# Performance work log

Measured on AMD Instinct MI355X. Metric: run time of the kernel, lower is better.

The kernel has to match this reference:

```python
import jax, jax.numpy as jnp
import numpy as np

N_NODES = 100000
NUM_REL = 2


def rgcn_conv(x, src, dst, etype, W, root, bias):
    """PyG-style RGCNConv: per-relation mean aggregation + root transform + bias.
    x: [N, in], W: [R, in, out], root: [in, out], bias: [out].
    """
    R = W.shape[0]
    N = x.shape[0]
    # Pre-transform nodes by every relation weight: [R, N, out]
    xr = jnp.einsum('ni,rio->rno', x, W)
    msgs = xr[etype, src]  # [E, out] gather per-edge, relation-typed
    seg_id = dst * R + etype  # combined (node, relation) segment id
    summed = jax.ops.segment_sum(msgs, seg_id, num_segments=N * R)
    cnt = jax.ops.segment_sum(jnp.ones(etype.shape, x.dtype), seg_id, num_segments=N * R)
    summed = summed.reshape(N, R, -1)
    cnt = cnt.reshape(N, R, 1)
    agg = (summed / jnp.maximum(cnt, 1.0)).sum(axis=1)  # sum over relations of per-relation means
    return agg + x @ root + bias


def setup_inputs() -> dict:
    key = jax.random.key(0)
    ks = jax.random.split(key, 9)
    d = 128
    E = 800000
    sc = 1.0 / np.sqrt(d)
    return {
        'x': jax.random.normal(ks[0], (N_NODES, d), jnp.float32),
        'edge_index_a': jax.random.randint(ks[1], (2, E), 0, N_NODES, jnp.int64),
        'edge_index_b': jax.random.randint(ks[2], (2, E), 0, N_NODES, jnp.int64),
        'W1': jax.random.normal(ks[3], (NUM_REL, d, d), jnp.float32) * sc,
        'root1': jax.random.normal(ks[4], (d, d), jnp.float32) * sc,
        'b1': jnp.zeros((d,), jnp.float32),
        'W2': jax.random.normal(ks[5], (NUM_REL, d, d), jnp.float32) * sc,
        'root2': jax.random.normal(ks[6], (d, d), jnp.float32) * sc,
        'b2': jnp.zeros((d,), jnp.float32),
    }


def reference(x, edge_index_a, edge_index_b, W1, root1, b1, W2, root2, b2):
    # Concatenate per-relation edge lists + build edge_type ids (a->0, b->1)
    edge_index = jnp.concatenate([edge_index_a, edge_index_b], axis=1)
    etype = jnp.concatenate([
        jnp.zeros((edge_index_a.shape[1],), jnp.int32),
        jnp.ones((edge_index_b.shape[1],), jnp.int32),
    ])
    src, dst = edge_index[0], edge_index[1]
    h = rgcn_conv(x, src, dst, etype, W1, root1, b1)
    h = jax.nn.relu(h)
    out = rgcn_conv(h, src, dst, etype, W2, root2, b2)
    return out
```

## Files before the change

kernel.cpp:

```cpp
#include <hip/hip_runtime.h>
#include <hip/hip_bf16.h>


typedef __attribute__((ext_vector_type(8))) short bf16x8;
typedef __attribute__((ext_vector_type(4))) float f32x4;
typedef unsigned short ushort_t;
typedef unsigned int uint_t;

#define BSHIFT 9
#define SEGB (1 << (BSHIFT + 1))
#define NBMAX 256
#define SLAB 16384
#define CH_PER_THREAD 8
#define CHUNK (256 * CH_PER_THREAD)
#define XSB 1024

#define GBM 256
#define KCH 128
#define LDBE 136

#define ROWB 768
#define XOFF 512

__device__ __forceinline__ ushort_t f2b(float f) {
  union { float f; uint_t u; } v;
  v.f = f;
  uint_t u = v.u;
  return (ushort_t)((u + 0x7FFFu + ((u >> 16) & 1u)) >> 16);
}
__device__ __forceinline__ void dot2acc(float& a, uint_t pk, uint_t sel) {
  asm("v_dot2_f32_bf16 %0, %1, %2, %0" : "+v"(a) : "v"(pk), "v"(sel));
}

__global__ __launch_bounds__(256) void prep_bin(
    const int* __restrict__ ea, const int* __restrict__ eb, int E, int NB,
    int* __restrict__ cursor, uint_t* __restrict__ staging, int nchunk,
    const float* __restrict__ W1, const float* __restrict__ root1,
    const float* __restrict__ W2, const float* __restrict__ root2,
    ushort_t* __restrict__ Bt1, ushort_t* __restrict__ Bt2,
    const float* __restrict__ x, ushort_t* __restrict__ aggbuf1, int N) {
  __shared__ int h[NBMAX];
  __shared__ int bbase[NBMAX];
  __shared__ int lofs[NBMAX];
  __shared__ int wtot[4];
  __shared__ uint_t sval[CHUNK];
  __shared__ int sdst[CHUNK];
  int b = blockIdx.x;
  int t = threadIdx.x;

  if (b < nchunk) {
    for (int i = t; i < NB; i += 256) h[i] = 0;
    __syncthreads();
    int base_i = b * CHUNK + t * CH_PER_THREAD;
    int total = 2 * E;
    int srcv[CH_PER_THREAD], dstv[CH_PER_THREAD], relv;
    bool valid8 = false;
    if (base_i + CH_PER_THREAD <= E) {
      int4 s0 = *(const int4*)(ea + base_i);
      int4 s1 = *(const int4*)(ea + base_i + 4);
      int4 d0 = *(const int4*)(ea + E + base_i);
      int4 d1 = *(const int4*)(ea + E + base_i + 4);
      srcv[0]=s0.x; srcv[1]=s0.y; srcv[2]=s0.z; srcv[3]=s0.w;
      srcv[4]=s1.x; srcv[5]=s1.y; srcv[6]=s1.z; srcv[7]=s1.w;
      dstv[0]=d0.x; dstv[1]=d0.y; dstv[2]=d0.z; dstv[3]=d0.w;
      dstv[4]=d1.x; dstv[5]=d1.y; dstv[6]=d1.z; dstv[7]=d1.w;
      relv = 0; valid8 = true;
    } else if (base_i >= E && base_i + CH_PER_THREAD <= total) {
      int off = base_i - E;
      int4 s0 = *(const int4*)(eb + off);
      int4 s1 = *(const int4*)(eb + off + 4);
      int4 d0 = *(const int4*)(eb + E + off);
      int4 d1 = *(const int4*)(eb + E + off + 4);
      srcv[0]=s0.x; srcv[1]=s0.y; srcv[2]=s0.z; srcv[3]=s0.w;
      srcv[4]=s1.x; srcv[5]=s1.y; srcv[6]=s1.z; srcv[7]=s1.w;
      dstv[0]=d0.x; dstv[1]=d0.y; dstv[2]=d0.z; dstv[3]=d0.w;
      dstv[4]=d1.x; dstv[5]=d1.y; dstv[6]=d1.z; dstv[7]=d1.w;
      relv = 1; valid8 = true;
    }
    uint_t val[CH_PER_THREAD];
    short bktv[CH_PER_THREAD];
    short rj[CH_PER_THREAD];
    if (valid8) {
#pragma unroll
      for (int j = 0; j < CH_PER_THREAD; ++j) {
        int seg = dstv[j] * 2 + relv;
        int bkt = seg >> (BSHIFT + 1);
        val[j] = ((uint_t)srcv[j] << 10) | (uint_t)(seg & (SEGB - 1));
        bktv[j] = (short)bkt;
        rj[j] = (short)atomicAdd(&h[bkt], 1);
      }
    } else {
#pragma unroll
      for (int j = 0; j < CH_PER_THREAD; ++j) {
        int i = base_i + j;
        if (i < total) {
          int src, dst, rel;
          if (i < E) { src = ea[i];     dst = ea[E + i]; rel = 0; }
          else       { src = eb[i - E]; dst = eb[i];     rel = 1; }
          int seg = dst * 2 + rel;
          int bkt = seg >> (BSHIFT + 1);
          val[j] = ((uint_t)src << 10) | (uint_t)(seg & (SEGB - 1));
          bktv[j] = (short)bkt;
          rj[j] = (short)atomicAdd(&h[bkt], 1);
        } else {
          bktv[j] = -1;
        }
      }
    }
    __syncthreads();
    {
      int v = (t < NB) ? h[t] : 0;
      int lane = t & 63, w = t >> 6;
      int s = v;
#pragma unroll
      for (int off = 1; off < 64; off <<= 1) {
        int u = __shfl_up(s, off);
        if (lane >= off) s += u;
      }
      if (lane == 63) wtot[w] = s;
      __syncthreads();
      int woff = 0;
#pragma unroll
      for (int i = 0; i < 4; ++i)
        if (i < w) woff += wtot[i];
      int incl = s + woff;
      if (t < NB) {
        lofs[t] = incl - v;
        bbase[t] = v ? t * SLAB + atomicAdd(&cursor[t], v) : 0;
      }
    }
    __syncthreads();
#pragma unroll
    for (int j = 0; j < CH_PER_THREAD; ++j) {
      if (!valid8 && bktv[j] < 0) continue;
      int bkt = bktv[j];
      int pos = lofs[bkt] + rj[j];
      sval[pos] = val[j];
      sdst[pos] = bbase[bkt] + rj[j];
    }
    __syncthreads();
    int nrec = 2 * E - b * CHUNK;
    if (nrec > CHUNK) nrec = CHUNK;
    for (int i = t; i < nrec; i += 256)
      staging[sdst[i]] = sval[i];
  } else if (b < nchunk + 384) {
    int flat = (b - nchunk) * 256 + t;
    int which = flat >= 49152;
    int idx = flat - which * 49152;
    int c = idx / 384;
    int k = idx - c * 384;
    const float* W = which ? W2 : W1;
    const float* root = which ? root2 : root1;
    ushort_t* Bt = which ? Bt2 : Bt1;
    float v = (k < 256) ? W[(size_t)k * 128 + c] : root[(size_t)(k - 256) * 128 + c];
    Bt[(size_t)c * 384 + k] = f2b(v);
  } else {
    int idx = (b - nchunk - 384) * 256 + t;
    int tot = N * 16;
    int step = XSB * 256;
    for (; idx < tot; idx += step) {
      int n = idx >> 4, tq = idx & 15;
      float4 a = *(const float4*)(x + (size_t)n * 128 + tq * 8);
      float4 c = *(const float4*)(x + (size_t)n * 128 + tq * 8 + 4);
      uint4 o;
      o.x = (uint_t)f2b(a.x) | ((uint_t)f2b(a.y) << 16);
      o.y = (uint_t)f2b(a.z) | ((uint_t)f2b(a.w) << 16);
      o.z = (uint_t)f2b(c.x) | ((uint_t)f2b(c.y) << 16);
      o.w = (uint_t)f2b(c.z) | ((uint_t)f2b(c.w) << 16);
      *(uint4*)(aggbuf1 + (size_t)n * 384 + 256 + tq * 8) = o;
    }
  }
}

__global__ __launch_bounds__(1024) void bucket_build(
    const uint_t* __restrict__ staging, const int* __restrict__ cursor,
    int* __restrict__ csr, int* __restrict__ offs,
    int* __restrict__ ends, int nseg) {
  __shared__ int scnt[SEGB];
  __shared__ int sexcl[SEGB];
  __shared__ int wtot[16];
  int b = blockIdx.x;
  int t = threadIdx.x;
  int base = b * SLAB;
  int ne = cursor[b];
  int seg0 = b << (BSHIFT + 1);

  scnt[t] = 0;
  __syncthreads();
  const uint_t* st = staging + base;
  uint_t rec[16];
  short rk[16];
#pragma unroll
  for (int k = 0; k < 4; ++k) {
    int i = (t + k * 1024) * 4;
    if (i + 4 <= ne) {
      uint4 v = *(const uint4*)(st + i);
      rec[k * 4 + 0] = v.x;
      rec[k * 4 + 1] = v.y;
      rec[k * 4 + 2] = v.z;
      rec[k * 4 + 3] = v.w;
#pragma unroll
      for (int j = 0; j < 4; ++j)
        rk[k * 4 + j] = (short)atomicAdd(&scnt[rec[k * 4 + j] & (SEGB - 1)], 1);
    } else {
#pragma unroll
      for (int j = 0; j < 4; ++j) {
        int i2 = i + j;
        if (i2 < ne) {
          uint_t v = st[i2];
          rec[k * 4 + j] = v;
          rk[k * 4 + j] = (short)atomicAdd(&scnt[v & (SEGB - 1)], 1);
        } else {
          rec[k * 4 + j] = 0xffffffffu;
        }
      }
    }
  }
  __syncthreads();
  int c = scnt[t];
  {
    int lane = t & 63, w = t >> 6;
    int s = c;
#pragma unroll
    for (int off = 1; off < 64; off <<= 1) {
      int u = __shfl_up(s, off);
      if (lane >= off) s += u;
    }
    if (lane == 63) wtot[w] = s;
    __syncthreads();
    int woff = 0;
#pragma unroll
    for (int i = 0; i < 16; ++i)
      if (i < w) woff += wtot[i];
    int excl = s + woff - c;
    sexcl[t] = excl;
    int g = seg0 + t;
    if (g < nseg) { offs[g] = base + excl; ends[g] = base + excl + c; }
  }
  __syncthreads();
#pragma unroll
  for (int k = 0; k < 16; ++k) {
    if (rec[k] != 0xffffffffu) {
      int seg = (int)(rec[k] & (SEGB - 1));
      int src = (int)(rec[k] >> 10);
      csr[base + sexcl[seg] + rk[k]] = src * ROWB + XOFF;
    }
  }
}

__global__ __launch_bounds__(256) void agg_kernel(
    const char* __restrict__ xbc,
    const int* __restrict__ csr,
    const int* __restrict__ offs, const int* __restrict__ ends,
    ushort_t* __restrict__ agg, int nseg) {
  int wid = (blockIdx.x * blockDim.x + threadIdx.x) >> 6;
  if (wid >= nseg) return;
  int lane = threadIdx.x & 63;
  int q = lane >> 4;
  int t = lane & 15;
  int beg = offs[wid], end = ends[wid];
  const uint_t sel_lo = 0x00003F80u;
  const uint_t sel_hi = 0x3F800000u;

  float acc[8];
#pragma unroll
  for (int j = 0; j < 8; ++j) acc[j] = 0.f;

  const char* xt = xbc + t * 16;
  int e = beg + q;
  for (; e + 4 < end; e += 8) {
    int o0 = csr[e];
    int o1 = csr[e + 4];
    uint4 v0 = *(const uint4*)(xt + o0);
    uint4 v1 = *(const uint4*)(xt + o1);
    dot2acc(acc[0], v0.x, sel_lo); dot2acc(acc[1], v0.x, sel_hi);
    dot2acc(acc[2], v0.y, sel_lo); dot2acc(acc[3], v0.y, sel_hi);
    dot2acc(acc[4], v0.z, sel_lo); dot2acc(acc[5], v0.z, sel_hi);
    dot2acc(acc[6], v0.w, sel_lo); dot2acc(acc[7], v0.w, sel_hi);
    dot2acc(acc[0], v1.x, sel_lo); dot2acc(acc[1], v1.x, sel_hi);
    dot2acc(acc[2], v1.y, sel_lo); dot2acc(acc[3], v1.y, sel_hi);
    dot2acc(acc[4], v1.z, sel_lo); dot2acc(acc[5], v1.z, sel_hi);
    dot2acc(acc[6], v1.w, sel_lo); dot2acc(acc[7], v1.w, sel_hi);
  }
  if (e < end) {
    int o0 = csr[e];
    uint4 v0 = *(const uint4*)(xt + o0);
    dot2acc(acc[0], v0.x, sel_lo); dot2acc(acc[1], v0.x, sel_hi);
    dot2acc(acc[2], v0.y, sel_lo); dot2acc(acc[3], v0.y, sel_hi);
    dot2acc(acc[4], v0.z, sel_lo); dot2acc(acc[5], v0.z, sel_hi);
    dot2acc(acc[6], v0.w, sel_lo); dot2acc(acc[7], v0.w, sel_hi);
  }

#pragma unroll
  for (int j = 0; j < 8; ++j) {
    acc[j] += __shfl_xor(acc[j], 16);
    acc[j] += __shfl_xor(acc[j], 32);
  }

  int c = end - beg;
  float inv = 1.0f / (float)(c > 1 ? c : 1);
  if (q == 0) {
    uint4 o;
    o.x = (uint_t)f2b(acc[0] * inv) | ((uint_t)f2b(acc[1] * inv) << 16);
    o.y = (uint_t)f2b(acc[2] * inv) | ((uint_t)f2b(acc[3] * inv) << 16);
    o.z = (uint_t)f2b(acc[4] * inv) | ((uint_t)f2b(acc[5] * inv) << 16);
    o.w = (uint_t)f2b(acc[6] * inv) | ((uint_t)f2b(acc[7] * inv) << 16);
    int n = wid >> 1, r = wid & 1;
    *(uint4*)(agg + (size_t)n * 384 + r * 128 + t * 8) = o;
  }
}

__device__ __forceinline__ void do_mfma32(
    const char* bs, f32x4 (&acc)[4][8], const bf16x8 (&a)[4],
    int ks, int lrow, int kg) {
  bf16x8 b[8];
#pragma unroll
  for (int c = 0; c < 8; ++c)
    b[c] = *(const bf16x8*)(bs + (c * 16 + lrow) * (LDBE * 2) +
                            (ks * 4 + kg) * 16);
#pragma unroll
  for (int r = 0; r < 4; ++r)
#pragma unroll
    for (int c = 0; c < 8; ++c)
      acc[r][c] = __builtin_amdgcn_mfma_f32_16x16x32_bf16(a[r], b[c], acc[r][c], 0, 0, 0);
}

template <int MODE>
__global__ __launch_bounds__(256, 2) void mfma_gemm(
    const ushort_t* __restrict__ A,
    const ushort_t* __restrict__ Bt,
    const float* __restrict__ bias,
    float* __restrict__ outf,
    ushort_t* __restrict__ outb,
    int M) {
  __shared__ __align__(16) ushort_t Bs[2][128 * LDBE];
  const int tid = threadIdx.x;
  const int lane = tid & 63;
  const int wave = tid >> 6;
  const int lrow = lane & 15;
  const int kg = lane >> 4;
  const int rowbase = blockIdx.x * GBM + wave * 64;

  f32x4 acc[4][8];
#pragma unroll
  for (int r = 0; r < 4; ++r)
#pragma unroll
    for (int c = 0; c < 8; ++c) acc[r][c] = (f32x4){0.f, 0.f, 0.f, 0.f};

  uint4 stg[8];
#pragma unroll
  for (int j = 0; j < 8; ++j) {
    int flat = tid + j * 256;
    int col = flat >> 4;
    int q = flat & 15;
    stg[j] = *(const uint4*)(Bt + (size_t)col * 384 + q * 8);
  }
#pragma unroll
  for (int j = 0; j < 8; ++j) {
    int flat = tid + j * 256;
    int col = flat >> 4;
    int q = flat & 15;
    *(uint4*)((char*)&Bs[0][0] + col * (LDBE * 2) + q * 16) = stg[j];
  }
  __syncthreads();

  int cur = 0;
  for (int ch = 0; ch < 3; ++ch) {
    if (ch < 2) {
#pragma unroll
      for (int j = 0; j < 8; ++j) {
        int flat = tid + j * 256;
        int col = flat >> 4;
        int q = flat & 15;
        stg[j] = *(const uint4*)(Bt + (size_t)col * 384 + (ch + 1) * KCH + q * 8);
      }
    }
    const ushort_t* ab = A + (size_t)ch * KCH + kg * 8;
    const char* bsbase = (const char*)&Bs[0][0] + cur * (128 * LDBE * 2);
    bf16x8 aA[4], aB[4];
#pragma unroll
    for (int r = 0; r < 4; ++r)
      aA[r] = *(const bf16x8*)(ab + (size_t)(rowbase + r * 16 + lrow) * 384);
#pragma unroll
    for (int r = 0; r < 4; ++r)
      aB[r] = *(const bf16x8*)(ab + (size_t)(rowbase + r * 16 + lrow) * 384 + 32);
    do_mfma32(bsbase, acc, aA, 0, lrow, kg);
#pragma unroll
    for (int r = 0; r < 4; ++r)
      aA[r] = *(const bf16x8*)(ab + (size_t)(rowbase + r * 16 + lrow) * 384 + 64);
    do_mfma32(bsbase, acc, aB, 1, lrow, kg);
#pragma unroll
    for (int r = 0; r < 4; ++r)
      aB[r] = *(const bf16x8*)(ab + (size_t)(rowbase + r * 16 + lrow) * 384 + 96);
    do_mfma32(bsbase, acc, aA, 2, lrow, kg);
    do_mfma32(bsbase, acc, aB, 3, lrow, kg);
    if (ch < 2) {
#pragma unroll
      for (int j = 0; j < 8; ++j) {
        int flat = tid + j * 256;
        int col = flat >> 4;
        int q = flat & 15;
        *(uint4*)((char*)&Bs[0][0] + (cur ^ 1) * (128 * LDBE * 2) +
                  col * (LDBE * 2) + q * 16) = stg[j];
      }
      __syncthreads();
      cur ^= 1;
    }
  }

  if (MODE == 1) {
    __syncthreads();
    ushort_t* ws = (ushort_t*)&Bs[0][0] + wave * (64 * 128);
#pragma unroll
    for (int c = 0; c < 8; ++c) {
      int col = c * 16 + lrow;
      float bv = bias[col];
#pragma unroll
      for (int r = 0; r < 4; ++r)
#pragma unroll
        for (int j = 0; j < 4; ++j) {
          float v = fmaxf(acc[r][c][j] + bv, 0.f);
          ws[(r * 16 + kg * 4 + j) * 128 + col] = f2b(v);
        }
    }
    __syncthreads();
#pragma unroll
    for (int rr = 0; rr < 16; ++rr) {
      int lr = rr * 4 + (lane >> 4);
      int row = rowbase + lr;
      int tq = lane & 15;
      if (row < M) {
        uint4 v = *(const uint4*)(ws + lr * 128 + tq * 8);
        *(uint4*)(outb + (size_t)row * 384 + 256 + tq * 8) = v;
      }
    }
  } else {
#pragma unroll
    for (int c = 0; c < 8; ++c) {
      int col = c * 16 + lrow;
      float bv = bias[col];
#pragma unroll
      for (int r = 0; r < 4; ++r) {
        int r0 = rowbase + r * 16 + kg * 4;
#pragma unroll
        for (int j = 0; j < 4; ++j) {
          int row = r0 + j;
          if (row < M) {
            outf[(size_t)row * 128 + col] = acc[r][c][j] + bv;
          }
        }
      }
    }
  }
}

extern "C" void kernel_launch(void* const* d_in, const int* in_sizes, int n_in,
                              void* d_out, int out_size, void* d_ws, size_t ws_size,
                              hipStream_t stream) {
  const float* x     = (const float*)d_in[0];
  const int*   ea    = (const int*)d_in[1];
  const int*   eb    = (const int*)d_in[2];
  const float* W1    = (const float*)d_in[3];
  const float* root1 = (const float*)d_in[4];
  const float* b1    = (const float*)d_in[5];
  const float* W2    = (const float*)d_in[6];
  const float* root2 = (const float*)d_in[7];
  const float* b2    = (const float*)d_in[8];
  float* out = (float*)d_out;

  const int N = in_sizes[0] / 128;
  const int E = in_sizes[1] / 2;
  const int nseg = N * 2;
  const int Mblk = (N + GBM - 1) / GBM;
  const int Mpad = Mblk * GBM;
  const int NB = ((N - 1) >> BSHIFT) + 1;
  const int nchunk = (2 * E + CHUNK - 1) / CHUNK;

  char* p = (char*)d_ws;
  ushort_t* aggbuf1 = (ushort_t*)p;  p += (size_t)Mpad * 384 * sizeof(ushort_t);
  ushort_t* aggbuf2 = (ushort_t*)p;  p += (size_t)Mpad * 384 * sizeof(ushort_t);
  ushort_t* Bt1 = (ushort_t*)p;      p += (size_t)128 * 384 * sizeof(ushort_t);
  ushort_t* Bt2 = (ushort_t*)p;      p += (size_t)128 * 384 * sizeof(ushort_t);
  int* csr = (int*)p;                p += (size_t)NBMAX * SLAB * sizeof(int);
  int* offs = (int*)p;               p += (size_t)nseg * sizeof(int);
  int* ends = (int*)p;               p += (size_t)nseg * sizeof(int);
  int* cursor = (int*)p;             p += NBMAX * sizeof(int);
  uint_t* staging = (uint_t*)aggbuf2;

  hipMemsetAsync(cursor, 0, NBMAX * sizeof(int), stream);

  prep_bin<<<nchunk + 384 + XSB, 256, 0, stream>>>(
      ea, eb, E, NB, cursor, staging, nchunk,
      W1, root1, W2, root2, Bt1, Bt2, x, aggbuf1, N);

  bucket_build<<<NB, 1024, 0, stream>>>(staging, cursor, csr, offs, ends, nseg);

  const int agg_blocks = (nseg + 3) / 4;

  agg_kernel<<<agg_blocks, 256, 0, stream>>>((const char*)aggbuf1, csr, offs,
                                             ends, aggbuf1, nseg);
  mfma_gemm<1><<<Mblk, 256, 0, stream>>>(aggbuf1, Bt1, b1, nullptr, aggbuf2, N);

  agg_kernel<<<agg_blocks, 256, 0, stream>>>((const char*)aggbuf2, csr, offs,
                                             ends, aggbuf2, nseg);
  mfma_gemm<0><<<Mblk, 256, 0, stream>>>(aggbuf2, Bt2, b2, out, nullptr, N);
}
```

Measured before the change: 288.2 us.

## Store activations in column-sliced layout so gathers hit a compact per-slice working set

Changes the bf16 activation/aggregation buffer from row-major [N,384] to 24 column slices of 16 features each, stored [slice][node][32 bytes]. The aggregation kernel now assigns each block to one slice, so concurrent blocks gather from a 3.2 MB slice that can stay cache-resident instead of scattering across the full 77 MB buffer. Each segment is now handled by 8 lanes instead of a 64-lane wave. The GEMM A-loads and epilogue stores are rewritten for the new layout. The cost is that each segment's CSR indices are re-read once per slice, and GEMM A-loads now stride across slices.

```diff
diff --git a/kernel.cpp b/kernel.cpp
--- a/kernel.cpp
+++ b/kernel.cpp
@@ -19,9 +19,6 @@
 #define KCH 128
 #define LDBE 136
 
-#define ROWB 768
-#define XOFF 512
-
 __device__ __forceinline__ ushort_t f2b(float f) {
   union { float f; uint_t u; } v;
   v.f = f;
@@ -31,6 +28,11 @@
 __device__ __forceinline__ void dot2acc(float& a, uint_t pk, uint_t sel) {
   asm("v_dot2_f32_bf16 %0, %1, %2, %0" : "+v"(a) : "v"(pk), "v"(sel));
 }
+#define ACC8(v)                                               \
+  dot2acc(acc[0], v.x, sel_lo); dot2acc(acc[1], v.x, sel_hi); \
+  dot2acc(acc[2], v.y, sel_lo); dot2acc(acc[3], v.y, sel_hi); \
+  dot2acc(acc[4], v.z, sel_lo); dot2acc(acc[5], v.z, sel_hi); \
+  dot2acc(acc[6], v.w, sel_lo); dot2acc(acc[7], v.w, sel_hi);
 
 __global__ __launch_bounds__(256) void prep_bin(
     const int* __restrict__ ea, const int* __restrict__ eb, int E, int NB,
@@ -38,7 +40,7 @@
     const float* __restrict__ W1, const float* __restrict__ root1,
     const float* __restrict__ W2, const float* __restrict__ root2,
     ushort_t* __restrict__ Bt1, ushort_t* __restrict__ Bt2,
-    const float* __restrict__ x, ushort_t* __restrict__ aggbuf1, int N) {
+    const float* __restrict__ x, char* __restrict__ A1, int N, int Mpad) {
   __shared__ int h[NBMAX];
   __shared__ int bbase[NBMAX];
   __shared__ int lofs[NBMAX];
@@ -155,6 +157,7 @@
     float v = (k < 256) ? W[(size_t)k * 128 + c] : root[(size_t)(k - 256) * 128 + c];
     Bt[(size_t)c * 384 + k] = f2b(v);
   } else {
+    size_t Mstride = (size_t)Mpad * 32;
     int idx = (b - nchunk - 384) * 256 + t;
     int tot = N * 16;
     int step = XSB * 256;
@@ -167,7 +170,8 @@
       o.y = (uint_t)f2b(a.z) | ((uint_t)f2b(a.w) << 16);
       o.z = (uint_t)f2b(c.x) | ((uint_t)f2b(c.y) << 16);
       o.w = (uint_t)f2b(c.z) | ((uint_t)f2b(c.w) << 16);
-      *(uint4*)(aggbuf1 + (size_t)n * 384 + 256 + tq * 8) = o;
+      *(uint4*)(A1 + (size_t)(16 + (tq >> 1)) * Mstride + (size_t)n * 32 +
+                (tq & 1) * 16) = o;
     }
   }
 }
@@ -243,22 +247,25 @@
     if (rec[k] != 0xffffffffu) {
       int seg = (int)(rec[k] & (SEGB - 1));
       int src = (int)(rec[k] >> 10);
-      csr[base + sexcl[seg] + rk[k]] = src * ROWB + XOFF;
+      csr[base + sexcl[seg] + rk[k]] = src * 32;
     }
   }
 }
 
 __global__ __launch_bounds__(256) void agg_kernel(
-    const char* __restrict__ xbc,
+    const char* __restrict__ Ain,
+    char* __restrict__ Aout,
     const int* __restrict__ csr,
     const int* __restrict__ offs, const int* __restrict__ ends,
-    ushort_t* __restrict__ agg, int nseg) {
-  int wid = (blockIdx.x * blockDim.x + threadIdx.x) >> 6;
-  if (wid >= nseg) return;
-  int lane = threadIdx.x & 63;
-  int q = lane >> 4;
-  int t = lane & 15;
-  int beg = offs[wid], end = ends[wid];
+    int nseg, int Mpad) {
+  size_t Mstride = (size_t)Mpad * 32;
+  int slice = blockIdx.x & 7;
+  int widx = (blockIdx.x >> 3) * 32 + (threadIdx.x >> 3);
+  if (widx >= nseg) return;
+  int l = threadIdx.x & 7;
+  int es = l >> 1;
+  int hb = l & 1;
+  int beg = offs[widx], end = ends[widx];
   const uint_t sel_lo = 0x00003F80u;
   const uint_t sel_hi = 0x3F800000u;
 
@@ -266,47 +273,38 @@
 #pragma unroll
   for (int j = 0; j < 8; ++j) acc[j] = 0.f;
 
-  const char* xt = xbc + t * 16;
-  int e = beg + q;
+  const char* xt = Ain + (size_t)(16 + slice) * Mstride + hb * 16;
+  int e = beg + es;
   for (; e + 4 < end; e += 8) {
     int o0 = csr[e];
     int o1 = csr[e + 4];
     uint4 v0 = *(const uint4*)(xt + o0);
     uint4 v1 = *(const uint4*)(xt + o1);
-    dot2acc(acc[0], v0.x, sel_lo); dot2acc(acc[1], v0.x, sel_hi);
-    dot2acc(acc[2], v0.y, sel_lo); dot2acc(acc[3], v0.y, sel_hi);
-    dot2acc(acc[4], v0.z, sel_lo); dot2acc(acc[5], v0.z, sel_hi);
-    dot2acc(acc[6], v0.w, sel_lo); dot2acc(acc[7], v0.w, sel_hi);
-    dot2acc(acc[0], v1.x, sel_lo); dot2acc(acc[1], v1.x, sel_hi);
-    dot2acc(acc[2], v1.y, sel_lo); dot2acc(acc[3], v1.y, sel_hi);
-    dot2acc(acc[4], v1.z, sel_lo); dot2acc(acc[5], v1.z, sel_hi);
-    dot2acc(acc[6], v1.w, sel_lo); dot2acc(acc[7], v1.w, sel_hi);
+    ACC8(v0); ACC8(v1);
   }
   if (e < end) {
     int o0 = csr[e];
     uint4 v0 = *(const uint4*)(xt + o0);
-    dot2acc(acc[0], v0.x, sel_lo); dot2acc(acc[1], v0.x, sel_hi);
-    dot2acc(acc[2], v0.y, sel_lo); dot2acc(acc[3], v0.y, sel_hi);
-    dot2acc(acc[4], v0.z, sel_lo); dot2acc(acc[5], v0.z, sel_hi);
-    dot2acc(acc[6], v0.w, sel_lo); dot2acc(acc[7], v0.w, sel_hi);
+    ACC8(v0);
   }
 
 #pragma unroll
   for (int j = 0; j < 8; ++j) {
-    acc[j] += __shfl_xor(acc[j], 16);
-    acc[j] += __shfl_xor(acc[j], 32);
+    acc[j] += __shfl_xor(acc[j], 2);
+    acc[j] += __shfl_xor(acc[j], 4);
   }
 
   int c = end - beg;
   float inv = 1.0f / (float)(c > 1 ? c : 1);
-  if (q == 0) {
+  if (es == 0) {
     uint4 o;
     o.x = (uint_t)f2b(acc[0] * inv) | ((uint_t)f2b(acc[1] * inv) << 16);
     o.y = (uint_t)f2b(acc[2] * inv) | ((uint_t)f2b(acc[3] * inv) << 16);
     o.z = (uint_t)f2b(acc[4] * inv) | ((uint_t)f2b(acc[5] * inv) << 16);
     o.w = (uint_t)f2b(acc[6] * inv) | ((uint_t)f2b(acc[7] * inv) << 16);
-    int n = wid >> 1, r = wid & 1;
-    *(uint4*)(agg + (size_t)n * 384 + r * 128 + t * 8) = o;
+    int n = widx >> 1, r = widx & 1;
+    *(uint4*)(Aout + (size_t)(r * 8 + slice) * Mstride + (size_t)n * 32 +
+              hb * 16) = o;
   }
 }
 
@@ -325,15 +323,21 @@
       acc[r][c] = __builtin_amdgcn_mfma_f32_16x16x32_bf16(a[r], b[c], acc[r][c], 0, 0, 0);
 }
 
+#define ALOAD(r, koff)                                                        \
+  (*(const bf16x8*)(Ap + (size_t)(((ch * KCH + (koff)) >> 4) + (kg >> 1)) *   \
+                             Mstride +                                        \
+                    (size_t)(rowbase + (r) * 16 + lrow) * 32 + (kg & 1) * 16))
+
 template <int MODE>
 __global__ __launch_bounds__(256, 2) void mfma_gemm(
-    const ushort_t* __restrict__ A,
+    const char* __restrict__ Ap,
     const ushort_t* __restrict__ Bt,
     const float* __restrict__ bias,
     float* __restrict__ outf,
-    ushort_t* __restrict__ outb,
-    int M) {
+    char* __restrict__ outb,
+    int M, int Mpad) {
   __shared__ __align__(16) ushort_t Bs[2][128 * LDBE];
+  size_t Mstride = (size_t)Mpad * 32;
   const int tid = threadIdx.x;
   const int lane = tid & 63;
   const int wave = tid >> 6;
@@ -375,23 +379,18 @@
         stg[j] = *(const uint4*)(Bt + (size_t)col * 384 + (ch + 1) * KCH + q * 8);
       }
     }
-    const ushort_t* ab = A + (size_t)ch * KCH + kg * 8;
     const char* bsbase = (const char*)&Bs[0][0] + cur * (128 * LDBE * 2);
     bf16x8 aA[4], aB[4];
 #pragma unroll
-    for (int r = 0; r < 4; ++r)
-      aA[r] = *(const bf16x8*)(ab + (size_t)(rowbase + r * 16 + lrow) * 384);
-#pragma unroll
-    for (int r = 0; r < 4; ++r)
-      aB[r] = *(const bf16x8*)(ab + (size_t)(rowbase + r * 16 + lrow) * 384 + 32);
+    for (int r = 0; r < 4; ++r) aA[r] = ALOAD(r, 0);
+#pragma unroll
+    for (int r = 0; r < 4; ++r) aB[r] = ALOAD(r, 32);
     do_mfma32(bsbase, acc, aA, 0, lrow, kg);
 #pragma unroll
-    for (int r = 0; r < 4; ++r)
-      aA[r] = *(const bf16x8*)(ab + (size_t)(rowbase + r * 16 + lrow) * 384 + 64);
+    for (int r = 0; r < 4; ++r) aA[r] = ALOAD(r, 64);
     do_mfma32(bsbase, acc, aB, 1, lrow, kg);
 #pragma unroll
-    for (int r = 0; r < 4; ++r)
-      aB[r] = *(const bf16x8*)(ab + (size_t)(rowbase + r * 16 + lrow) * 384 + 96);
+    for (int r = 0; r < 4; ++r) aB[r] = ALOAD(r, 96);
     do_mfma32(bsbase, acc, aA, 2, lrow, kg);
     do_mfma32(bsbase, acc, aB, 3, lrow, kg);
     if (ch < 2) {
@@ -431,7 +430,8 @@
       int tq = lane & 15;
       if (row < M) {
         uint4 v = *(const uint4*)(ws + lr * 128 + tq * 8);
-        *(uint4*)(outb + (size_t)row * 384 + 256 + tq * 8) = v;
+        *(uint4*)(outb + (size_t)(16 + (tq >> 1)) * Mstride +
+                  (size_t)row * 32 + (tq & 1) * 16) = v;
       }
     }
   } else {
@@ -477,31 +477,29 @@
   const int nchunk = (2 * E + CHUNK - 1) / CHUNK;
 
   char* p = (char*)d_ws;
-  ushort_t* aggbuf1 = (ushort_t*)p;  p += (size_t)Mpad * 384 * sizeof(ushort_t);
-  ushort_t* aggbuf2 = (ushort_t*)p;  p += (size_t)Mpad * 384 * sizeof(ushort_t);
+  char* A1 = p;                      p += (size_t)Mpad * 768;
+  char* A2 = p;                      p += (size_t)Mpad * 768;
   ushort_t* Bt1 = (ushort_t*)p;      p += (size_t)128 * 384 * sizeof(ushort_t);
   ushort_t* Bt2 = (ushort_t*)p;      p += (size_t)128 * 384 * sizeof(ushort_t);
   int* csr = (int*)p;                p += (size_t)NBMAX * SLAB * sizeof(int);
   int* offs = (int*)p;               p += (size_t)nseg * sizeof(int);
   int* ends = (int*)p;               p += (size_t)nseg * sizeof(int);
   int* cursor = (int*)p;             p += NBMAX * sizeof(int);
-  uint_t* staging = (uint_t*)aggbuf2;
+  uint_t* staging = (uint_t*)A2;
 
   hipMemsetAsync(cursor, 0, NBMAX * sizeof(int), stream);
 
   prep_bin<<<nchunk + 384 + XSB, 256, 0, stream>>>(
       ea, eb, E, NB, cursor, staging, nchunk,
-      W1, root1, W2, root2, Bt1, Bt2, x, aggbuf1, N);
+      W1, root1, W2, root2, Bt1, Bt2, x, A1, N, Mpad);
 
   bucket_build<<<NB, 1024, 0, stream>>>(staging, cursor, csr, offs, ends, nseg);
 
-  const int agg_blocks = (nseg + 3) / 4;
-
-  agg_kernel<<<agg_blocks, 256, 0, stream>>>((const char*)aggbuf1, csr, offs,
-                                             ends, aggbuf1, nseg);
-  mfma_gemm<1><<<Mblk, 256, 0, stream>>>(aggbuf1, Bt1, b1, nullptr, aggbuf2, N);
-
-  agg_kernel<<<agg_blocks, 256, 0, stream>>>((const char*)aggbuf2, csr, offs,
-                                             ends, aggbuf2, nseg);
-  mfma_gemm<0><<<Mblk, 256, 0, stream>>>(aggbuf2, Bt2, b2, out, nullptr, N);
-}
+  const int agg_blocks = 8 * ((nseg + 31) / 32);
+
+  agg_kernel<<<agg_blocks, 256, 0, stream>>>(A1, A1, csr, offs, ends, nseg, Mpad);
+  mfma_gemm<1><<<Mblk, 256, 0, stream>>>(A1, Bt1, b1, nullptr, A2, N, Mpad);
+
+  agg_kernel<<<agg_blocks, 256, 0, stream>>>(A2, A2, csr, offs, ends, nseg, Mpad);
+  mfma_gemm<0><<<Mblk, 256, 0, stream>>>(A2, Bt2, b2, out, nullptr, N, Mpad);
+}
```

After: 311.8 us. 1.08x slower.
